# Optimization experiments

Hardware: AMD Instinct MI355X
Metric: run time of the kernel (lower is better)

The kernel has to match this reference:

```python
import jax, jax.numpy as jnp
import numpy as np

N, E = 384, 3072          # nodes, relation pairs
CIN, EMB, D = 4096, 200, 512  # roi feat dim, glove dim, hidden dim
NOBJ, NREL = 151, 51
NUM_ITER = 3
ALPHA = 0.5


def setup_inputs() -> dict:
    key = jax.random.key(0)
    ks = iter(jax.random.split(key, 64))

    def w(shape, scale=0.02):
        return jax.random.normal(next(ks), shape, dtype=jnp.float32) * scale

    inp = {
        'x': jax.random.normal(next(ks), (N, CIN), dtype=jnp.float32),
        'pos_info': jax.random.uniform(next(ks), (N, 9), dtype=jnp.float32),
        'union_features': jax.random.normal(next(ks), (E, CIN), dtype=jnp.float32),
        'obj_labels': jax.random.randint(next(ks), (N,), 0, NOBJ, dtype=jnp.int32),
        'rel_pair_idx': jax.random.randint(next(ks), (E, 2), 0, N, dtype=jnp.int32),
        # embeddings
        'obj_embed1_w': w((NOBJ, EMB)),
        'obj_embed2_w': w((NOBJ, EMB)),
        # node/edge embeddings
        'node_emb_w': w((D, CIN + EMB + 128)), 'node_emb_b': jnp.zeros((D,)),
        'node_emb2_w': w((D, CIN + EMB + D)), 'node_emb2_b': jnp.zeros((D,)),
        'edge_emb_w': w((D, CIN)), 'edge_emb_b': jnp.zeros((D,)),
        # pos_embed: Linear(9,32) -> BN(32) -> Linear(32,128) -> ReLU
        'pos_w1': w((32, 9)), 'pos_b1': jnp.zeros((32,)),
        'pos_gamma': jnp.ones((32,)), 'pos_beta': jnp.zeros((32,)),
        'pos_w2': w((128, 32)), 'pos_b2': jnp.zeros((128,)),
        # node GRUCell (with bias), edge GRUCell (no bias); gate order r,z,n
        'ngate_wih': w((3 * D, D)), 'ngate_whh': w((3 * D, D)),
        'ngate_bih': jnp.zeros((3 * D,)), 'ngate_bhh': jnp.zeros((3 * D,)),
        'egate_wih': w((3 * D, D)), 'egate_whh': w((3 * D, D)),
        # message kernels
        'n2n_w1': w((D, D)), 'n2n_b1': jnp.zeros((D,)),
        'n2n_w2': w((D, D)), 'n2n_b2': jnp.zeros((D,)),
        'e2n_w1': w((D, D)), 'e2n_b1': jnp.zeros((D,)),
        'e2n_w2': w((D, D)), 'e2n_b2': jnp.zeros((D,)),
        # node2edge 1x1 convs == pointwise linears
        'n2e_w1': w((D, 2 * D)), 'n2e_b1': jnp.zeros((D,)),
        'n2e_w2': w((D, D)), 'n2e_b2': jnp.zeros((D,)),
        'rel_cls_w': w((NREL, D)), 'rel_cls_b': jnp.zeros((NREL,)),
    }
    return inp


def _gru(x, h, wih, whh, bih=None, bhh=None):
    gi = x @ wih.T
    gh = h @ whh.T
    if bih is not None:
        gi = gi + bih
        gh = gh + bhh
    ir, iz, ig = jnp.split(gi, 3, axis=-1)
    hr, hz, hg = jnp.split(gh, 3, axis=-1)
    r = jax.nn.sigmoid(ir + hr)
    z = jax.nn.sigmoid(iz + hz)
    g = jnp.tanh(ig + r * hg)
    return (1.0 - z) * g + z * h


def _mlp2(h, w1, b1, w2, b2):
    h = jax.nn.relu(h @ w1.T + b1)
    return jax.nn.relu(h @ w2.T + b2)


def reference(x, pos_info, union_features, obj_labels, rel_pair_idx,
              obj_embed1_w, obj_embed2_w,
              node_emb_w, node_emb_b, node_emb2_w, node_emb2_b,
              edge_emb_w, edge_emb_b,
              pos_w1, pos_b1, pos_gamma, pos_beta, pos_w2, pos_b2,
              ngate_wih, ngate_whh, ngate_bih, ngate_bhh,
              egate_wih, egate_whh,
              n2n_w1, n2n_b1, n2n_w2, n2n_b2,
              e2n_w1, e2n_b1, e2n_w2, e2n_b2,
              n2e_w1, n2e_b1, n2e_w2, n2e_b2,
              rel_cls_w, rel_cls_b):
    n = x.shape[0]
    # pos embed (BatchNorm in training mode = batch stats)
    ph = pos_info @ pos_w1.T + pos_b1
    mu, var = ph.mean(0), ph.var(0)
    ph = (ph - mu) * jax.lax.rsqrt(var + 1e-5) * pos_gamma + pos_beta
    pos_embed = jax.nn.relu(ph @ pos_w2.T + pos_b2)

    obj_embed = obj_embed1_w[obj_labels]  # predcls: GT labels
    node_states = jnp.concatenate([x, obj_embed, pos_embed], -1) @ node_emb_w.T + node_emb_b

    p0, p1 = rel_pair_idx[:, 0], rel_pair_idx[:, 1]
    adj = jnp.zeros((n, n), jnp.float32).at[p0, p1].set(1.0)
    edge_rep = union_features @ edge_emb_w.T + edge_emb_b
    # torch sparse to_dense sums duplicate indices
    edge_states = jnp.zeros((n, n, D), jnp.float32).at[p0, p1].add(edge_rep)

    deg = adj.sum(1, keepdims=True) + 1e-6
    for _ in range(NUM_ITER):
        n2n = (adj @ node_states) / deg
        e2n = jnp.einsum('ij,ijd->jd', adj, edge_states)
        n2n = _mlp2(n2n, n2n_w1, n2n_b1, n2n_w2, n2n_b2)
        e2n = _mlp2(e2n, e2n_w1, e2n_b1, e2n_w2, e2n_b2)
        node_states = _gru(ALPHA * n2n + (1.0 - ALPHA) * e2n, node_states,
                           ngate_wih, ngate_whh, ngate_bih, ngate_bhh)

    # predcls: obj_dists = to_onehot(labels), preds = labels
    obj_dists = jnp.full((n, NOBJ), -1000.0, jnp.float32).at[jnp.arange(n), obj_labels].set(1000.0)
    node_states = jnp.concatenate([x, node_states, obj_embed2_w[obj_labels]], -1) @ node_emb2_w.T + node_emb2_b

    for _ in range(NUM_ITER):
        # all-pairs direction-aware concat, masked by adjacency
        ek = jnp.concatenate([
            jnp.broadcast_to(node_states[:, None, :], (n, n, D)),
            jnp.broadcast_to(node_states[None, :, :], (n, n, D)),
        ], -1) * adj[:, :, None]                      # [n, n, 2D]
        msg = _mlp2(ek, n2e_w1, n2e_b1, n2e_w2, n2e_b2)  # 1x1 convs == pointwise
        edge_states = _gru(msg.reshape(n * n, D), edge_states.reshape(n * n, D),
                           egate_wih, egate_whh).reshape(n, n, D)

    rel_feats = edge_states[p0, p1]
    rel_dists = rel_feats @ rel_cls_w.T + rel_cls_b
    return obj_dists, rel_dists
```

## Files before the change

kernel.cpp:

```cpp
#include <hip/hip_runtime.h>

typedef unsigned short ushort_t;
typedef unsigned int uint_t;

#define N_    384
#define E_    3072
#define CIN_  4096
#define EMB_  200
#define D_    512
#define NOBJ_ 151
#define NREL_ 51
#define K1_   (CIN_ + EMB_ + 128)
#define K1P_  4448
#define K2_   (CIN_ + EMB_ + D_)
#define K2P_  4832

__device__ __forceinline__ ushort_t f2b(float f) {
    uint_t u = __float_as_uint(f);
    u += 0x7FFFu + ((u >> 16) & 1u);
    return (ushort_t)(u >> 16);
}

__global__ void k_pair_min(const int* __restrict__ rp, int* __restrict__ mapMin) {
    int e = blockIdx.x * blockDim.x + threadIdx.x;
    if (e >= E_) return;
    atomicMin(&mapMin[rp[2 * e] * N_ + rp[2 * e + 1]], e);
}
__global__ void k_pair_rep(const int* __restrict__ rp, const int* __restrict__ mapMin,
                           int* __restrict__ rep, int* __restrict__ deg_cnt) {
    int e = blockIdx.x * blockDim.x + threadIdx.x;
    if (e >= E_) return;
    int r = mapMin[rp[2 * e] * N_ + rp[2 * e + 1]];
    rep[e] = r;
    if (r == e) atomicAdd(&deg_cnt[rp[2 * e]], 1);
}
__global__ void k_inv_deg(const int* __restrict__ deg_cnt, float* __restrict__ inv_deg) {
    int i = blockIdx.x * blockDim.x + threadIdx.x;
    if (i < N_) inv_deg[i] = 1.0f / ((float)deg_cnt[i] + 1e-6f);
}

__global__ __launch_bounds__(1024) void k_pos_a(const float* __restrict__ pi,
                                                const float* __restrict__ w1,
                                                const float* __restrict__ b1,
                                                const float* __restrict__ g,
                                                const float* __restrict__ be,
                                                float* __restrict__ posn) {
    __shared__ float ph[N_ * 32];
    __shared__ float mu_s[32], rs_s[32];
    int tid = threadIdx.x;
    for (int idx = tid; idx < N_ * 32; idx += 1024) {
        int i = idx >> 5, f = idx & 31;
        float s = b1[f];
        for (int k = 0; k < 9; ++k) s += pi[i * 9 + k] * w1[f * 9 + k];
        ph[idx] = s;
    }
    __syncthreads();
    if (tid < 32) {
        float s = 0.f;
        for (int i = 0; i < N_; ++i) s += ph[i * 32 + tid];
        float m = s / N_;
        float v = 0.f;
        for (int i = 0; i < N_; ++i) { float d = ph[i * 32 + tid] - m; v += d * d; }
        mu_s[tid] = m;
        rs_s[tid] = rsqrtf(v / N_ + 1e-5f);
    }
    __syncthreads();
    for (int idx = tid; idx < N_ * 32; idx += 1024) {
        int f = idx & 31;
        posn[idx] = (ph[idx] - mu_s[f]) * rs_s[f] * g[f] + be[f];
    }
}
__global__ void k_pos2(const float* __restrict__ pn, const float* __restrict__ w,
                       const float* __restrict__ b, float* __restrict__ out) {
    int idx = blockIdx.x * blockDim.x + threadIdx.x;
    if (idx >= N_ * 128) return;
    int i = idx / 128, f = idx % 128;
    float s = b[f];
    for (int k = 0; k < 32; ++k) s += pn[i * 32 + k] * w[f * 32 + k];
    out[idx] = fmaxf(s, 0.f);
}

__global__ void k_build_A1b(const float* __restrict__ x, const int* __restrict__ lab,
                            const float* __restrict__ emb1, const float* __restrict__ pe,
                            ushort_t* __restrict__ A) {
    int idx = blockIdx.x * blockDim.x + threadIdx.x;
    if (idx >= N_ * K1P_) return;
    int i = idx / K1P_, c = idx % K1P_;
    float v = 0.f;
    if (c < CIN_)             v = x[(size_t)i * CIN_ + c];
    else if (c < CIN_ + EMB_) v = emb1[lab[i] * EMB_ + (c - CIN_)];
    else if (c < K1_)         v = pe[i * 128 + (c - CIN_ - EMB_)];
    A[idx] = f2b(v);
}
__global__ void k_build_A2b(const float* __restrict__ x, const int* __restrict__ lab,
                            const float* __restrict__ emb2, const float* __restrict__ ns,
                            ushort_t* __restrict__ A) {
    int idx = blockIdx.x * blockDim.x + threadIdx.x;
    if (idx >= N_ * K2P_) return;
    int i = idx / K2P_, c = idx % K2P_;
    float v = 0.f;
    if (c < CIN_)             v = x[(size_t)i * CIN_ + c];
    else if (c < CIN_ + D_)   v = ns[i * D_ + (c - CIN_)];
    else if (c < K2_)         v = emb2[lab[i] * EMB_ + (c - CIN_ - D_)];
    A[idx] = f2b(v);
}
__global__ void k_build_ekb(const int* __restrict__ rp, const float* __restrict__ ns,
                            ushort_t* __restrict__ ek) {
    int idx = blockIdx.x * blockDim.x + threadIdx.x;
    if (idx >= E_ * 2 * D_) return;
    int e = idx / (2 * D_), c = idx % (2 * D_);
    float v = (c < D_) ? ns[rp[2 * e] * D_ + c] : ns[rp[2 * e + 1] * D_ + (c - D_)];
    ek[idx] = f2b(v);
}

struct ConvDesc { const float* src; ushort_t* dst; int K, Kp, rows, rowsp; };
struct ConvArgs { ConvDesc d[16]; };
__global__ void k_conv_batch(ConvArgs a) {
    ConvDesc c = a.d[blockIdx.y];
    for (int row = blockIdx.x; row < c.rowsp; row += gridDim.x) {
        const float* src = c.src + (size_t)row * c.K;
        ushort_t* dst = c.dst + (size_t)row * c.Kp;
        bool inrow = row < c.rows;
        for (int k = threadIdx.x * 4; k < c.Kp; k += blockDim.x * 4) {
            uint2 ov = {0u, 0u};
            if (inrow && k < c.K) {
                float4 v = *(const float4*)(src + k);
                ov.x = (uint_t)f2b(v.x) | ((uint_t)f2b(v.y) << 16);
                ov.y = (uint_t)f2b(v.z) | ((uint_t)f2b(v.w) << 16);
            }
            *(uint2*)(dst + k) = ov;
        }
    }
}
__global__ void k_f2b_n(const float* __restrict__ s, ushort_t* __restrict__ d, int n) {
    int i = blockIdx.x * blockDim.x + threadIdx.x;
    if (i < n) d[i] = f2b(s[i]);
}

__global__ void k_scatter_edge(const float* __restrict__ er, const int* __restrict__ rep,
                               float* __restrict__ es) {
    int e = blockIdx.x;
    int d = blockIdx.y * 256 + threadIdx.x;
    atomicAdd(&es[(size_t)rep[e] * D_ + d], er[(size_t)e * D_ + d]);
}
__global__ void k_broadcast_es(const int* __restrict__ rep, float* __restrict__ es,
                               ushort_t* __restrict__ esb) {
    int idx = blockIdx.x * blockDim.x + threadIdx.x;
    if (idx >= E_ * D_) return;
    int e = idx / D_, d = idx % D_;
    float v = es[(size_t)rep[e] * D_ + d];
    es[idx] = v;
    esb[idx] = f2b(v);
}
__global__ void k_scatter_e2n(const int* __restrict__ rp, const int* __restrict__ rep,
                              const float* __restrict__ es, float* __restrict__ e2n) {
    int e = blockIdx.x;
    if (rep[e] != e) return;
    int d = blockIdx.y * 256 + threadIdx.x;
    atomicAdd(&e2n[rp[2 * e + 1] * D_ + d], es[(size_t)e * D_ + d]);
}
__global__ void k_scatter_n2n(const int* __restrict__ rp, const int* __restrict__ rep,
                              const float* __restrict__ ns, float* __restrict__ n2n) {
    int e = blockIdx.x;
    if (rep[e] != e) return;
    int d = blockIdx.y * 256 + threadIdx.x;
    atomicAdd(&n2n[rp[2 * e] * D_ + d], ns[rp[2 * e + 1] * D_ + d]);
}
__global__ void k_scale_rows_b(const float* __restrict__ a, const float* __restrict__ inv_deg,
                               ushort_t* __restrict__ ob) {
    int idx = blockIdx.x * blockDim.x + threadIdx.x;
    if (idx >= N_ * D_) return;
    ob[idx] = f2b(a[idx] * inv_deg[idx / D_]);
}
__global__ void k_combine_b(const float* __restrict__ a, const float* __restrict__ b,
                            ushort_t* __restrict__ o) {
    int idx = blockIdx.x * blockDim.x + threadIdx.x;
    if (idx >= N_ * D_) return;
    o[idx] = f2b(0.5f * a[idx] + 0.5f * b[idx]);
}
__global__ void k_gru(const float* __restrict__ gi, const float* __restrict__ gh,
                      const float* __restrict__ bih, const float* __restrict__ bhh,
                      float* __restrict__ h, ushort_t* __restrict__ hb, int M) {
    int idx = blockIdx.x * blockDim.x + threadIdx.x;
    if (idx >= M * D_) return;
    int m = idx / D_, d = idx % D_;
    size_t b3 = (size_t)m * 3 * D_;
    float ir = gi[b3 + d], iz = gi[b3 + D_ + d], ig = gi[b3 + 2 * D_ + d];
    float hr = gh[b3 + d], hz = gh[b3 + D_ + d], hg = gh[b3 + 2 * D_ + d];
    if (bih) { ir += bih[d]; iz += bih[D_ + d]; ig += bih[2 * D_ + d]; }
    if (bhh) { hr += bhh[d]; hz += bhh[D_ + d]; hg += bhh[2 * D_ + d]; }
    float r = 1.f / (1.f + expf(-(ir + hr)));
    float z = 1.f / (1.f + expf(-(iz + hz)));
    float g = tanhf(ig + r * hg);
    size_t hi = (size_t)m * D_ + d;
    float nv = (1.f - z) * g + z * h[hi];
    h[hi] = nv;
    if (hb) hb[hi] = f2b(nv);
}
__global__ void k_obj_dists(const int* __restrict__ lab, float* __restrict__ out) {
    int idx = blockIdx.x * blockDim.x + threadIdx.x;
    if (idx >= N_ * NOBJ_) return;
    out[idx] = (idx % NOBJ_ == lab[idx / NOBJ_]) ? 1000.f : -1000.f;
}

typedef __attribute__((ext_vector_type(8))) short sh8;
typedef __attribute__((ext_vector_type(4))) float f32x4;

#define GLOAD_LDS16(gp, lp)                                                        \
    __builtin_amdgcn_global_load_lds((__attribute__((address_space(1))) void*)(gp),\
                                     (__attribute__((address_space(3))) void*)(lp),\
                                     16, 0, 0)

template <int FM, int FN>
__device__ __forceinline__ void gemm_body(ushort_t* As, ushort_t* Bs,
                                          const ushort_t* __restrict__ A,
                                          const ushort_t* __restrict__ B,
                                          const float* __restrict__ bias,
                                          float* __restrict__ C,
                                          ushort_t* __restrict__ Cb,
                                          int M, int N, int K, int relu,
                                          int bx, int by) {
    constexpr int BM = FM * 32, BN = FN * 32;
    constexpr int ATILES = (BM + 63) / 64, BTILES = (BN + 63) / 64;
    const int tid = threadIdx.x;
    const int lane = tid & 63, wid = tid >> 6;
    const int wr = wid >> 1, wc = wid & 1;
    const int bm = by * BM, bn = bx * BN;
    const int ar = tid >> 2, ac = (tid & 3) * 8;
    const int l15 = lane & 15, lg = lane >> 4;

    f32x4 acc[FM][FN];
#pragma unroll
    for (int m = 0; m < FM; ++m)
#pragma unroll
        for (int n = 0; n < FN; ++n) acc[m][n] = (f32x4){0.f, 0.f, 0.f, 0.f};

    for (int k0 = 0; k0 < K; k0 += 32) {
#pragma unroll
        for (int i = 0; i < ATILES; ++i) {
            int r = i * 64 + ar;
            if ((BM & 63) == 0 || r < BM)
                GLOAD_LDS16(A + (size_t)(bm + r) * K + k0 + ac, &As[r * 32 + ac]);
        }
#pragma unroll
        for (int i = 0; i < BTILES; ++i) {
            int r = i * 64 + ar;
            if ((BN & 63) == 0 || r < BN)
                GLOAD_LDS16(B + (size_t)(bn + r) * K + k0 + ac, &Bs[r * 32 + ac]);
        }
        __syncthreads();
        sh8 af[FM], bf[FN];
#pragma unroll
        for (int m = 0; m < FM; ++m)
            af[m] = *(const sh8*)&As[(wr * FM * 16 + m * 16 + l15) * 32 + lg * 8];
#pragma unroll
        for (int n = 0; n < FN; ++n)
            bf[n] = *(const sh8*)&Bs[(wc * FN * 16 + n * 16 + l15) * 32 + lg * 8];
#pragma unroll
        for (int m = 0; m < FM; ++m)
#pragma unroll
            for (int n = 0; n < FN; ++n)
                acc[m][n] = __builtin_amdgcn_mfma_f32_16x16x32_bf16(af[m], bf[n], acc[m][n], 0, 0, 0);
        __syncthreads();
    }

    const int r0 = bm + wr * FM * 16, c0 = bn + wc * FN * 16;
#pragma unroll
    for (int m = 0; m < FM; ++m)
#pragma unroll
        for (int n = 0; n < FN; ++n)
#pragma unroll
            for (int j = 0; j < 4; ++j) {
                int row = r0 + m * 16 + lg * 4 + j;
                int col = c0 + n * 16 + l15;
                if (row < M && col < N) {
                    float v = acc[m][n][j] + (bias ? bias[col] : 0.f);
                    if (relu) v = fmaxf(v, 0.f);
                    if (C)  C[(size_t)row * N + col] = v;
                    if (Cb) Cb[(size_t)row * N + col] = f2b(v);
                }
            }
}

template <int FM, int FN>
__global__ __launch_bounds__(256) void gemm_mfma(const ushort_t* __restrict__ A,
                                                 const ushort_t* __restrict__ B,
                                                 const float* __restrict__ bias,
                                                 float* __restrict__ C,
                                                 ushort_t* __restrict__ Cb,
                                                 int M, int N, int K, int relu) {
    __shared__ ushort_t As[FM * 32 * 32];
    __shared__ ushort_t Bs[FN * 32 * 32];
    gemm_body<FM, FN>(As, Bs, A, B, bias, C, Cb, M, N, K, relu, blockIdx.x, blockIdx.y);
}

__global__ __launch_bounds__(256) void gemm_dual11(const ushort_t* __restrict__ A0,
                                                   const ushort_t* __restrict__ B0,
                                                   float* __restrict__ C0,
                                                   const ushort_t* __restrict__ A1,
                                                   const ushort_t* __restrict__ B1,
                                                   float* __restrict__ C1,
                                                   int M, int N, int K) {
    __shared__ ushort_t As[32 * 32];
    __shared__ ushort_t Bs[32 * 32];
    if (blockIdx.z == 0)
        gemm_body<1, 1>(As, Bs, A0, B0, nullptr, C0, nullptr, M, N, K, 0, blockIdx.x, blockIdx.y);
    else
        gemm_body<1, 1>(As, Bs, A1, B1, nullptr, C1, nullptr, M, N, K, 0, blockIdx.x, blockIdx.y);
}

static inline dim3 mgrid(int M, int N, int FM, int FN) {
    return dim3((N + FN * 32 - 1) / (FN * 32), (M + FM * 32 - 1) / (FM * 32));
}

extern "C" void kernel_launch(void* const* d_in, const int* in_sizes, int n_in,
                              void* d_out, int out_size, void* d_ws, size_t ws_size,
                              hipStream_t stream) {
    const float* x      = (const float*)d_in[0];
    const float* posi   = (const float*)d_in[1];
    const float* unionf = (const float*)d_in[2];
    const int*   lab    = (const int*)d_in[3];
    const int*   rp     = (const int*)d_in[4];
    const float* emb1   = (const float*)d_in[5];
    const float* emb2   = (const float*)d_in[6];
    const float* nw     = (const float*)d_in[7];
    const float* nb     = (const float*)d_in[8];
    const float* nw2    = (const float*)d_in[9];
    const float* nb2    = (const float*)d_in[10];
    const float* ew     = (const float*)d_in[11];
    const float* eb     = (const float*)d_in[12];
    const float* pw1    = (const float*)d_in[13];
    const float* pb1    = (const float*)d_in[14];
    const float* pg     = (const float*)d_in[15];
    const float* pbe    = (const float*)d_in[16];
    const float* pw2    = (const float*)d_in[17];
    const float* pb2    = (const float*)d_in[18];
    const float* ngwih  = (const float*)d_in[19];
    const float* ngwhh  = (const float*)d_in[20];
    const float* ngbih  = (const float*)d_in[21];
    const float* ngbhh  = (const float*)d_in[22];
    const float* egwih  = (const float*)d_in[23];
    const float* egwhh  = (const float*)d_in[24];
    const float* n2nw1  = (const float*)d_in[25];
    const float* n2nb1  = (const float*)d_in[26];
    const float* n2nw2  = (const float*)d_in[27];
    const float* n2nb2  = (const float*)d_in[28];
    const float* e2nw1  = (const float*)d_in[29];
    const float* e2nb1  = (const float*)d_in[30];
    const float* e2nw2  = (const float*)d_in[31];
    const float* e2nb2  = (const float*)d_in[32];
    const float* n2ew1  = (const float*)d_in[33];
    const float* n2eb1  = (const float*)d_in[34];
    const float* n2ew2  = (const float*)d_in[35];
    const float* n2eb2  = (const float*)d_in[36];
    const float* relw   = (const float*)d_in[37];
    const float* relb   = (const float*)d_in[38];

    size_t off = 0;
    auto alloc = [&](size_t bytes) {
        off = (off + 255) & ~(size_t)255;
        char* p = (char*)d_ws + off;
        off += bytes;
        return (void*)p;
    };
    int*      mapMin  = (int*)alloc((size_t)N_ * N_ * 4);
    int*      rep     = (int*)alloc(E_ * 4);
    int*      deg_cnt = (int*)alloc(N_ * 4);
    float*    inv_deg = (float*)alloc(N_ * 4);
    float*    posn    = (float*)alloc(N_ * 32 * 4);
    float*    pe      = (float*)alloc(N_ * 128 * 4);
    float*    ns      = (float*)alloc((size_t)N_ * D_ * 4);
    ushort_t* nsb     = (ushort_t*)alloc((size_t)N_ * D_ * 2);
    char*     unionU  = (char*)alloc((size_t)E_ * 2 * D_ * 2);
    ushort_t* A1b = (ushort_t*)unionU;
    ushort_t* A2b = (ushort_t*)unionU;
    ushort_t* ekb = (ushort_t*)unionU;
    char*     ufbU = (char*)alloc((size_t)E_ * CIN_ * 2);
    ushort_t* ufb = (ushort_t*)ufbU;
    float*    gie = (float*)ufbU;
    char*     erepU = (char*)alloc((size_t)E_ * D_ * 4);
    float*    erep  = (float*)erepU;
    ushort_t* erepb = (ushort_t*)erepU;
    ushort_t* msgb  = (ushort_t*)(erepU + (size_t)E_ * D_ * 2);
    float*    es    = (float*)alloc((size_t)E_ * D_ * 4);
    ushort_t* esb   = (ushort_t*)alloc((size_t)E_ * D_ * 2);
    float*    e2n   = (float*)alloc((size_t)N_ * D_ * 4);
    ushort_t* e2nb  = (ushort_t*)alloc((size_t)N_ * D_ * 2);
    ushort_t* tmpb  = (ushort_t*)alloc((size_t)N_ * D_ * 2);
    float*    e2nm  = (float*)alloc((size_t)N_ * D_ * 4);
    float*    n2n   = (float*)alloc((size_t)N_ * D_ * 4);
    ushort_t* n2nb  = (ushort_t*)alloc((size_t)N_ * D_ * 2);
    float*    n2nm  = (float*)alloc((size_t)N_ * D_ * 4);
    ushort_t* xinb  = (ushort_t*)alloc((size_t)N_ * D_ * 2);
    char*     gheU = (char*)alloc((size_t)E_ * 3 * D_ * 4);
    float*    ghe = (float*)gheU;
    float*    gin = (float*)gheU;
    float*    ghn = (float*)(gheU + (size_t)N_ * 3 * D_ * 4);
    ushort_t* nwb     = (ushort_t*)alloc((size_t)D_ * K1P_ * 2);
    ushort_t* nw2b    = (ushort_t*)alloc((size_t)D_ * K2P_ * 2);
    ushort_t* ewb     = (ushort_t*)alloc((size_t)D_ * CIN_ * 2);
    ushort_t* ngwihb  = (ushort_t*)alloc((size_t)3 * D_ * D_ * 2);
    ushort_t* ngwhhb  = (ushort_t*)alloc((size_t)3 * D_ * D_ * 2);
    ushort_t* egwihb  = (ushort_t*)alloc((size_t)3 * D_ * D_ * 2);
    ushort_t* egwhhb  = (ushort_t*)alloc((size_t)3 * D_ * D_ * 2);
    ushort_t* n2nw1b  = (ushort_t*)alloc((size_t)D_ * D_ * 2);
    ushort_t* n2nw2b  = (ushort_t*)alloc((size_t)D_ * D_ * 2);
    ushort_t* e2nw1b  = (ushort_t*)alloc((size_t)D_ * D_ * 2);
    ushort_t* e2nw2b  = (ushort_t*)alloc((size_t)D_ * D_ * 2);
    ushort_t* n2ew1b  = (ushort_t*)alloc((size_t)D_ * 2 * D_ * 2);
    ushort_t* n2ew2b  = (ushort_t*)alloc((size_t)D_ * D_ * 2);
    ushort_t* relwb   = (ushort_t*)alloc((size_t)64 * D_ * 2);
    if (off > ws_size) return;

    float* out_obj = (float*)d_out;
    float* out_rel = (float*)d_out + N_ * NOBJ_;

    ConvArgs ca;
    int ci = 0;
    auto addc = [&](const float* s, ushort_t* dptr, int K, int Kp, int rows, int rowsp) {
        ca.d[ci++] = ConvDesc{s, dptr, K, Kp, rows, rowsp};
    };
    addc(nw,    nwb,    K1_,      K1P_,     D_,       D_);
    addc(nw2,   nw2b,   K2_,      K2P_,     D_,       D_);
    addc(ew,    ewb,    CIN_,     CIN_,     D_,       D_);
    addc(ngwih, ngwihb, D_,       D_,       3 * D_,   3 * D_);
    addc(ngwhh, ngwhhb, D_,       D_,       3 * D_,   3 * D_);
    addc(egwih, egwihb, D_,       D_,       3 * D_,   3 * D_);
    addc(egwhh, egwhhb, D_,       D_,       3 * D_,   3 * D_);
    addc(n2nw1, n2nw1b, D_,       D_,       D_,       D_);
    addc(n2nw2, n2nw2b, D_,       D_,       D_,       D_);
    addc(e2nw1, e2nw1b, D_,       D_,       D_,       D_);
    addc(e2nw2, e2nw2b, D_,       D_,       D_,       D_);
    addc(n2ew1, n2ew1b, 2 * D_,   2 * D_,   D_,       D_);
    addc(n2ew2, n2ew2b, D_,       D_,       D_,       D_);
    addc(relw,  relwb,  D_,       D_,       NREL_,    64);
    addc(unionf, ufb,   CIN_,     CIN_,     E_,       E_);
    for (; ci < 16;) ca.d[ci++] = ConvDesc{nullptr, nullptr, 4, 4, 0, 0};
    k_conv_batch<<<dim3(512, 15), 256, 0, stream>>>(ca);

    (void)hipMemsetAsync(mapMin, 0x7F, (size_t)N_ * N_ * 4, stream);
    (void)hipMemsetAsync(deg_cnt, 0, N_ * 4, stream);
    k_pair_min<<<(E_ + 255) / 256, 256, 0, stream>>>(rp, mapMin);
    k_pair_rep<<<(E_ + 255) / 256, 256, 0, stream>>>(rp, mapMin, rep, deg_cnt);
    k_inv_deg<<<(N_ + 255) / 256, 256, 0, stream>>>(deg_cnt, inv_deg);

    k_pos_a<<<1, 1024, 0, stream>>>(posi, pw1, pb1, pg, pbe, posn);
    k_pos2<<<(N_ * 128 + 255) / 256, 256, 0, stream>>>(posn, pw2, pb2, pe);

    k_build_A1b<<<((size_t)N_ * K1P_ + 255) / 256, 256, 0, stream>>>(x, lab, emb1, pe, A1b);
    gemm_mfma<1, 1><<<mgrid(N_, D_, 1, 1), 256, 0, stream>>>(A1b, nwb, nb, ns, nsb, N_, D_, K1P_, 0);

    gemm_mfma<2, 2><<<mgrid(E_, D_, 2, 2), 256, 0, stream>>>(ufb, ewb, eb, erep, nullptr, E_, D_, CIN_, 0);
    (void)hipMemsetAsync(es, 0, (size_t)E_ * D_ * 4, stream);
    k_scatter_edge<<<dim3(E_, 2), 256, 0, stream>>>(erep, rep, es);
    k_broadcast_es<<<(E_ * D_ + 255) / 256, 256, 0, stream>>>(rep, es, esb);

    (void)hipMemsetAsync(e2n, 0, (size_t)N_ * D_ * 4, stream);
    k_scatter_e2n<<<dim3(E_, 2), 256, 0, stream>>>(rp, rep, es, e2n);
    k_f2b_n<<<(N_ * D_ + 255) / 256, 256, 0, stream>>>(e2n, e2nb, N_ * D_);
    gemm_mfma<1, 1><<<mgrid(N_, D_, 1, 1), 256, 0, stream>>>(e2nb, e2nw1b, e2nb1, nullptr, tmpb, N_, D_, D_, 1);
    gemm_mfma<1, 1><<<mgrid(N_, D_, 1, 1), 256, 0, stream>>>(tmpb, e2nw2b, e2nb2, e2nm, nullptr, N_, D_, D_, 1);

    for (int it = 0; it < 3; ++it) {
        (void)hipMemsetAsync(n2n, 0, (size_t)N_ * D_ * 4, stream);
        k_scatter_n2n<<<dim3(E_, 2), 256, 0, stream>>>(rp, rep, ns, n2n);
        k_scale_rows_b<<<(N_ * D_ + 255) / 256, 256, 0, stream>>>(n2n, inv_deg, n2nb);
        gemm_mfma<1, 1><<<mgrid(N_, D_, 1, 1), 256, 0, stream>>>(n2nb, n2nw1b, n2nb1, nullptr, tmpb, N_, D_, D_, 1);
        gemm_mfma<1, 1><<<mgrid(N_, D_, 1, 1), 256, 0, stream>>>(tmpb, n2nw2b, n2nb2, n2nm, nullptr, N_, D_, D_, 1);
        k_combine_b<<<(N_ * D_ + 255) / 256, 256, 0, stream>>>(n2nm, e2nm, xinb);
        {
            dim3 g = mgrid(N_, 3 * D_, 1, 1);
            gemm_dual11<<<dim3(g.x, g.y, 2), 256, 0, stream>>>(xinb, ngwihb, gin, nsb, ngwhhb, ghn, N_, 3 * D_, D_);
        }
        k_gru<<<(N_ * D_ + 255) / 256, 256, 0, stream>>>(gin, ghn, ngbih, ngbhh, ns, nsb, N_);
    }

    k_obj_dists<<<(N_ * NOBJ_ + 255) / 256, 256, 0, stream>>>(lab, out_obj);

    k_build_A2b<<<((size_t)N_ * K2P_ + 255) / 256, 256, 0, stream>>>(x, lab, emb2, ns, A2b);
    gemm_mfma<1, 1><<<mgrid(N_, D_, 1, 1), 256, 0, stream>>>(A2b, nw2b, nb2, ns, nsb, N_, D_, K2P_, 0);

    k_build_ekb<<<((size_t)E_ * 2 * D_ + 255) / 256, 256, 0, stream>>>(rp, ns, ekb);
    gemm_mfma<2, 2><<<mgrid(E_, D_, 2, 2), 256, 0, stream>>>(ekb, n2ew1b, n2eb1, nullptr, erepb, E_, D_, 2 * D_, 1);
    gemm_mfma<2, 2><<<mgrid(E_, D_, 2, 2), 256, 0, stream>>>(erepb, n2ew2b, n2eb2, nullptr, msgb, E_, D_, D_, 1);
    gemm_mfma<2, 4><<<mgrid(E_, 3 * D_, 2, 4), 256, 0, stream>>>(msgb, egwihb, nullptr, gie, nullptr, E_, 3 * D_, D_, 0);
    for (int it = 0; it < 3; ++it) {
        gemm_mfma<2, 4><<<mgrid(E_, 3 * D_, 2, 4), 256, 0, stream>>>(esb, egwhhb, nullptr, ghe, nullptr, E_, 3 * D_, D_, 0);
        k_gru<<<(E_ * D_ + 255) / 256, 256, 0, stream>>>(gie, ghe, nullptr, nullptr, es, esb, E_);
    }

    gemm_mfma<1, 1><<<mgrid(E_, NREL_, 1, 1), 256, 0, stream>>>(esb, relwb, relb, out_rel, nullptr, E_, NREL_, D_, 0);
}
```

Baseline: 728.0 us.

## Apply split-K with atomic accumulation to small-M node GEMMs and add epilogue kernels

Replaces the single-pass GEMMs for the node-side linears (N=384 rows), the edge embedding, the GRU gate projections and the relation classifier with a split-K variant. Each K-slice block atomically adds its partial sum into a zeroed fp32 buffer, and separate epilogue kernels then apply bias and ReLU and write the bf16 copy. The goal is more blocks for GEMMs whose grids were too small to fill the GPU. The cost is extra memsets, fp32 atomics, extra launches and non-deterministic summation order.

```diff
diff --git a/kernel.cpp b/kernel.cpp
--- a/kernel.cpp
+++ b/kernel.cpp
@@ -172,11 +172,29 @@
     if (idx >= N_ * D_) return;
     ob[idx] = f2b(a[idx] * inv_deg[idx / D_]);
 }
-__global__ void k_combine_b(const float* __restrict__ a, const float* __restrict__ b,
-                            ushort_t* __restrict__ o) {
+__global__ void k_combine_b(const float* __restrict__ araw, const float* __restrict__ b2,
+                            const float* __restrict__ e2nm, ushort_t* __restrict__ o) {
     int idx = blockIdx.x * blockDim.x + threadIdx.x;
     if (idx >= N_ * D_) return;
-    o[idx] = f2b(0.5f * a[idx] + 0.5f * b[idx]);
+    float a = fmaxf(araw[idx] + b2[idx & (D_ - 1)], 0.f);
+    o[idx] = f2b(0.5f * a + 0.5f * e2nm[idx]);
+}
+__global__ void k_epi(const float* __restrict__ raw, const float* __restrict__ bias,
+                      float* __restrict__ fo, ushort_t* __restrict__ bo,
+                      int total, int colmask, int relu) {
+    int idx = blockIdx.x * blockDim.x + threadIdx.x;
+    if (idx >= total) return;
+    float v = raw[idx] + bias[idx & colmask];
+    if (relu) v = fmaxf(v, 0.f);
+    if (fo) fo[idx] = v;
+    if (bo) bo[idx] = f2b(v);
+}
+__global__ void k_epi_rel(const float* __restrict__ raw, const float* __restrict__ relb,
+                          float* __restrict__ out) {
+    int idx = blockIdx.x * blockDim.x + threadIdx.x;
+    if (idx >= E_ * NREL_) return;
+    int row = idx / NREL_, col = idx % NREL_;
+    out[idx] = raw[row * 64 + col] + relb[col];
 }
 __global__ void k_gru(const float* __restrict__ gi, const float* __restrict__ gh,
                       const float* __restrict__ bih, const float* __restrict__ bhh,
@@ -212,30 +230,20 @@
                                      16, 0, 0)
 
 template <int FM, int FN>
-__device__ __forceinline__ void gemm_body(ushort_t* As, ushort_t* Bs,
-                                          const ushort_t* __restrict__ A,
-                                          const ushort_t* __restrict__ B,
-                                          const float* __restrict__ bias,
-                                          float* __restrict__ C,
-                                          ushort_t* __restrict__ Cb,
-                                          int M, int N, int K, int relu,
-                                          int bx, int by) {
+__device__ __forceinline__ void gemm_kloop(ushort_t* As, ushort_t* Bs,
+                                           const ushort_t* __restrict__ A,
+                                           const ushort_t* __restrict__ B,
+                                           f32x4 (&acc)[FM][FN],
+                                           int K, int ks0, int ks1, int bm, int bn) {
     constexpr int BM = FM * 32, BN = FN * 32;
     constexpr int ATILES = (BM + 63) / 64, BTILES = (BN + 63) / 64;
     const int tid = threadIdx.x;
     const int lane = tid & 63, wid = tid >> 6;
     const int wr = wid >> 1, wc = wid & 1;
-    const int bm = by * BM, bn = bx * BN;
     const int ar = tid >> 2, ac = (tid & 3) * 8;
     const int l15 = lane & 15, lg = lane >> 4;
-
-    f32x4 acc[FM][FN];
-#pragma unroll
-    for (int m = 0; m < FM; ++m)
-#pragma unroll
-        for (int n = 0; n < FN; ++n) acc[m][n] = (f32x4){0.f, 0.f, 0.f, 0.f};
-
-    for (int k0 = 0; k0 < K; k0 += 32) {
+    for (int ks = ks0; ks < ks1; ++ks) {
+        int k0 = ks * 32;
 #pragma unroll
         for (int i = 0; i < ATILES; ++i) {
             int r = i * 64 + ar;
@@ -263,8 +271,27 @@
                 acc[m][n] = __builtin_amdgcn_mfma_f32_16x16x32_bf16(af[m], bf[n], acc[m][n], 0, 0, 0);
         __syncthreads();
     }
-
-    const int r0 = bm + wr * FM * 16, c0 = bn + wc * FN * 16;
+}
+
+template <int FM, int FN>
+__global__ __launch_bounds__(256) void gemm_mfma(const ushort_t* __restrict__ A,
+                                                 const ushort_t* __restrict__ B,
+                                                 const float* __restrict__ bias,
+                                                 float* __restrict__ C,
+                                                 ushort_t* __restrict__ Cb,
+                                                 int M, int N, int K, int relu) {
+    __shared__ ushort_t As[FM * 32 * 32];
+    __shared__ ushort_t Bs[FN * 32 * 32];
+    const int bm = blockIdx.y * FM * 32, bn = blockIdx.x * FN * 32;
+    f32x4 acc[FM][FN];
+#pragma unroll
+    for (int m = 0; m < FM; ++m)
+#pragma unroll
+        for (int n = 0; n < FN; ++n) acc[m][n] = (f32x4){0.f, 0.f, 0.f, 0.f};
+    gemm_kloop<FM, FN>(As, Bs, A, B, acc, K, 0, K / 32, bm, bn);
+    const int lane = threadIdx.x & 63, wid = threadIdx.x >> 6;
+    const int l15 = lane & 15, lg = lane >> 4;
+    const int r0 = bm + (wid >> 1) * FM * 16, c0 = bn + (wid & 1) * FN * 16;
 #pragma unroll
     for (int m = 0; m < FM; ++m)
 #pragma unroll
@@ -283,34 +310,46 @@
 }
 
 template <int FM, int FN>
-__global__ __launch_bounds__(256) void gemm_mfma(const ushort_t* __restrict__ A,
-                                                 const ushort_t* __restrict__ B,
-                                                 const float* __restrict__ bias,
-                                                 float* __restrict__ C,
-                                                 ushort_t* __restrict__ Cb,
-                                                 int M, int N, int K, int relu) {
+__global__ __launch_bounds__(256) void gemm_splitk(const ushort_t* __restrict__ A,
+                                                   const ushort_t* __restrict__ B,
+                                                   float* __restrict__ C,
+                                                   int M, int N, int K, int S) {
     __shared__ ushort_t As[FM * 32 * 32];
     __shared__ ushort_t Bs[FN * 32 * 32];
-    gemm_body<FM, FN>(As, Bs, A, B, bias, C, Cb, M, N, K, relu, blockIdx.x, blockIdx.y);
-}
-
-__global__ __launch_bounds__(256) void gemm_dual11(const ushort_t* __restrict__ A0,
-                                                   const ushort_t* __restrict__ B0,
-                                                   float* __restrict__ C0,
-                                                   const ushort_t* __restrict__ A1,
-                                                   const ushort_t* __restrict__ B1,
-                                                   float* __restrict__ C1,
-                                                   int M, int N, int K) {
-    __shared__ ushort_t As[32 * 32];
-    __shared__ ushort_t Bs[32 * 32];
-    if (blockIdx.z == 0)
-        gemm_body<1, 1>(As, Bs, A0, B0, nullptr, C0, nullptr, M, N, K, 0, blockIdx.x, blockIdx.y);
-    else
-        gemm_body<1, 1>(As, Bs, A1, B1, nullptr, C1, nullptr, M, N, K, 0, blockIdx.x, blockIdx.y);
+    const int nsteps = K / 32;
+    const int ss = (nsteps + S - 1) / S;
+    const int ks0 = blockIdx.z * ss;
+    const int ks1 = min(nsteps, ks0 + ss);
+    if (ks0 >= ks1) return;
+    const int bm = blockIdx.y * FM * 32, bn = blockIdx.x * FN * 32;
+    f32x4 acc[FM][FN];
+#pragma unroll
+    for (int m = 0; m < FM; ++m)
+#pragma unroll
+        for (int n = 0; n < FN; ++n) acc[m][n] = (f32x4){0.f, 0.f, 0.f, 0.f};
+    gemm_kloop<FM, FN>(As, Bs, A, B, acc, K, ks0, ks1, bm, bn);
+    const int lane = threadIdx.x & 63, wid = threadIdx.x >> 6;
+    const int l15 = lane & 15, lg = lane >> 4;
+    const int r0 = bm + (wid >> 1) * FM * 16, c0 = bn + (wid & 1) * FN * 16;
+#pragma unroll
+    for (int m = 0; m < FM; ++m)
+#pragma unroll
+        for (int n = 0; n < FN; ++n)
+#pragma unroll
+            for (int j = 0; j < 4; ++j) {
+                int row = r0 + m * 16 + lg * 4 + j;
+                int col = c0 + n * 16 + l15;
+                if (row < M && col < N)
+                    atomicAdd(&C[(size_t)row * N + col], acc[m][n][j]);
+            }
 }
 
 static inline dim3 mgrid(int M, int N, int FM, int FN) {
     return dim3((N + FN * 32 - 1) / (FN * 32), (M + FM * 32 - 1) / (FM * 32));
+}
+static inline dim3 sgrid(int M, int N, int FM, int FN, int S) {
+    dim3 g = mgrid(M, N, FM, FN);
+    return dim3(g.x, g.y, S);
 }
 
 extern "C" void kernel_launch(void* const* d_in, const int* in_sizes, int n_in,
@@ -371,6 +410,16 @@
     float*    pe      = (float*)alloc(N_ * 128 * 4);
     float*    ns      = (float*)alloc((size_t)N_ * D_ * 4);
     ushort_t* nsb     = (ushort_t*)alloc((size_t)N_ * D_ * 2);
+    float*    nsraw   = (float*)alloc((size_t)N_ * D_ * 4);
+    char*     scrR    = (char*)alloc((size_t)(2 * N_ * D_ + N_ * D_ + 2 * N_ * 3 * D_) * 4);
+    float*    n2n     = (float*)scrR;
+    float*    tmpraw  = (float*)(scrR + (size_t)N_ * D_ * 4);
+    float*    n2nmraw = (float*)(scrR + (size_t)2 * N_ * D_ * 4);
+    float*    gin     = (float*)(scrR + (size_t)3 * N_ * D_ * 4);
+    float*    ghn     = (float*)(scrR + (size_t)(3 * N_ * D_ + N_ * 3 * D_) * 4);
+    const size_t scrBytes = (size_t)(3 * N_ * D_ + 2 * N_ * 3 * D_) * 4;
+    float*    e2nm    = (float*)alloc((size_t)N_ * D_ * 4);
+    float*    relraw  = (float*)alloc((size_t)E_ * 64 * 4);
     char*     unionU  = (char*)alloc((size_t)E_ * 2 * D_ * 2);
     ushort_t* A1b = (ushort_t*)unionU;
     ushort_t* A2b = (ushort_t*)unionU;
@@ -387,15 +436,9 @@
     float*    e2n   = (float*)alloc((size_t)N_ * D_ * 4);
     ushort_t* e2nb  = (ushort_t*)alloc((size_t)N_ * D_ * 2);
     ushort_t* tmpb  = (ushort_t*)alloc((size_t)N_ * D_ * 2);
-    float*    e2nm  = (float*)alloc((size_t)N_ * D_ * 4);
-    float*    n2n   = (float*)alloc((size_t)N_ * D_ * 4);
     ushort_t* n2nb  = (ushort_t*)alloc((size_t)N_ * D_ * 2);
-    float*    n2nm  = (float*)alloc((size_t)N_ * D_ * 4);
     ushort_t* xinb  = (ushort_t*)alloc((size_t)N_ * D_ * 2);
-    char*     gheU = (char*)alloc((size_t)E_ * 3 * D_ * 4);
-    float*    ghe = (float*)gheU;
-    float*    gin = (float*)gheU;
-    float*    ghn = (float*)(gheU + (size_t)N_ * 3 * D_ * 4);
+    float*    ghe   = (float*)alloc((size_t)E_ * 3 * D_ * 4);
     ushort_t* nwb     = (ushort_t*)alloc((size_t)D_ * K1P_ * 2);
     ushort_t* nw2b    = (ushort_t*)alloc((size_t)D_ * K2P_ * 2);
     ushort_t* ewb     = (ushort_t*)alloc((size_t)D_ * CIN_ * 2);
@@ -448,9 +491,13 @@
     k_pos2<<<(N_ * 128 + 255) / 256, 256, 0, stream>>>(posn, pw2, pb2, pe);
 
     k_build_A1b<<<((size_t)N_ * K1P_ + 255) / 256, 256, 0, stream>>>(x, lab, emb1, pe, A1b);
-    gemm_mfma<1, 1><<<mgrid(N_, D_, 1, 1), 256, 0, stream>>>(A1b, nwb, nb, ns, nsb, N_, D_, K1P_, 0);
-
-    gemm_mfma<2, 2><<<mgrid(E_, D_, 2, 2), 256, 0, stream>>>(ufb, ewb, eb, erep, nullptr, E_, D_, CIN_, 0);
+    (void)hipMemsetAsync(nsraw, 0, (size_t)N_ * D_ * 4, stream);
+    gemm_splitk<1, 1><<<sgrid(N_, D_, 1, 1, 8), 256, 0, stream>>>(A1b, nwb, nsraw, N_, D_, K1P_, 8);
+    k_epi<<<(N_ * D_ + 255) / 256, 256, 0, stream>>>(nsraw, nb, ns, nsb, N_ * D_, D_ - 1, 0);
+
+    (void)hipMemsetAsync(erep, 0, (size_t)E_ * D_ * 4, stream);
+    gemm_splitk<2, 2><<<sgrid(E_, D_, 2, 2, 2), 256, 0, stream>>>(ufb, ewb, erep, E_, D_, CIN_, 2);
+    k_epi<<<((size_t)E_ * D_ + 255) / 256, 256, 0, stream>>>(erep, eb, erep, nullptr, E_ * D_, D_ - 1, 0);
     (void)hipMemsetAsync(es, 0, (size_t)E_ * D_ * 4, stream);
     k_scatter_edge<<<dim3(E_, 2), 256, 0, stream>>>(erep, rep, es);
     k_broadcast_es<<<(E_ * D_ + 255) / 256, 256, 0, stream>>>(rep, es, esb);
@@ -458,27 +505,31 @@
     (void)hipMemsetAsync(e2n, 0, (size_t)N_ * D_ * 4, stream);
     k_scatter_e2n<<<dim3(E_, 2), 256, 0, stream>>>(rp, rep, es, e2n);
     k_f2b_n<<<(N_ * D_ + 255) / 256, 256, 0, stream>>>(e2n, e2nb, N_ * D_);
-    gemm_mfma<1, 1><<<mgrid(N_, D_, 1, 1), 256, 0, stream>>>(e2nb, e2nw1b, e2nb1, nullptr, tmpb, N_, D_, D_, 1);
-    gemm_mfma<1, 1><<<mgrid(N_, D_, 1, 1), 256, 0, stream>>>(tmpb, e2nw2b, e2nb2, e2nm, nullptr, N_, D_, D_, 1);
+    (void)hipMemsetAsync(scrR, 0, scrBytes, stream);
+    gemm_splitk<1, 1><<<sgrid(N_, D_, 1, 1, 8), 256, 0, stream>>>(e2nb, e2nw1b, tmpraw, N_, D_, D_, 8);
+    k_epi<<<(N_ * D_ + 255) / 256, 256, 0, stream>>>(tmpraw, e2nb1, nullptr, tmpb, N_ * D_, D_ - 1, 1);
+    gemm_splitk<1, 1><<<sgrid(N_, D_, 1, 1, 8), 256, 0, stream>>>(tmpb, e2nw2b, n2nmraw, N_, D_, D_, 8);
+    k_epi<<<(N_ * D_ + 255) / 256, 256, 0, stream>>>(n2nmraw, e2nb2, e2nm, nullptr, N_ * D_, D_ - 1, 1);
 
     for (int it = 0; it < 3; ++it) {
-        (void)hipMemsetAsync(n2n, 0, (size_t)N_ * D_ * 4, stream);
+        (void)hipMemsetAsync(scrR, 0, scrBytes, stream);
         k_scatter_n2n<<<dim3(E_, 2), 256, 0, stream>>>(rp, rep, ns, n2n);
         k_scale_rows_b<<<(N_ * D_ + 255) / 256, 256, 0, stream>>>(n2n, inv_deg, n2nb);
-        gemm_mfma<1, 1><<<mgrid(N_, D_, 1, 1), 256, 0, stream>>>(n2nb, n2nw1b, n2nb1, nullptr, tmpb, N_, D_, D_, 1);
-        gemm_mfma<1, 1><<<mgrid(N_, D_, 1, 1), 256, 0, stream>>>(tmpb, n2nw2b, n2nb2, n2nm, nullptr, N_, D_, D_, 1);
-        k_combine_b<<<(N_ * D_ + 255) / 256, 256, 0, stream>>>(n2nm, e2nm, xinb);
-        {
-            dim3 g = mgrid(N_, 3 * D_, 1, 1);
-            gemm_dual11<<<dim3(g.x, g.y, 2), 256, 0, stream>>>(xinb, ngwihb, gin, nsb, ngwhhb, ghn, N_, 3 * D_, D_);
-        }
+        gemm_splitk<1, 1><<<sgrid(N_, D_, 1, 1, 8), 256, 0, stream>>>(n2nb, n2nw1b, tmpraw, N_, D_, D_, 8);
+        k_epi<<<(N_ * D_ + 255) / 256, 256, 0, stream>>>(tmpraw, n2nb1, nullptr, tmpb, N_ * D_, D_ - 1, 1);
+        gemm_splitk<1, 1><<<sgrid(N_, D_, 1, 1, 8), 256, 0, stream>>>(tmpb, n2nw2b, n2nmraw, N_, D_, D_, 8);
+        k_combine_b<<<(N_ * D_ + 255) / 256, 256, 0, stream>>>(n2nmraw, n2nb2, e2nm, xinb);
+        gemm_splitk<1, 1><<<sgrid(N_, 3 * D_, 1, 1, 4), 256, 0, stream>>>(xinb, ngwihb, gin, N_, 3 * D_, D_, 4);
+        gemm_splitk<1, 1><<<sgrid(N_, 3 * D_, 1, 1, 4), 256, 0, stream>>>(nsb, ngwhhb, ghn, N_, 3 * D_, D_, 4);
         k_gru<<<(N_ * D_ + 255) / 256, 256, 0, stream>>>(gin, ghn, ngbih, ngbhh, ns, nsb, N_);
     }
 
     k_obj_dists<<<(N_ * NOBJ_ + 255) / 256, 256, 0, stream>>>(lab, out_obj);
 
     k_build_A2b<<<((size_t)N_ * K2P_ + 255) / 256, 256, 0, stream>>>(x, lab, emb2, ns, A2b);
-    gemm_mfma<1, 1><<<mgrid(N_, D_, 1, 1), 256, 0, stream>>>(A2b, nw2b, nb2, ns, nsb, N_, D_, K2P_, 0);
+    (void)hipMemsetAsync(nsraw, 0, (size_t)N_ * D_ * 4, stream);
+    gemm_splitk<1, 1><<<sgrid(N_, D_, 1, 1, 8), 256, 0, stream>>>(A2b, nw2b, nsraw, N_, D_, K2P_, 8);
+    k_epi<<<(N_ * D_ + 255) / 256, 256, 0, stream>>>(nsraw, nb2, ns, nsb, N_ * D_, D_ - 1, 0);
 
     k_build_ekb<<<((size_t)E_ * 2 * D_ + 255) / 256, 256, 0, stream>>>(rp, ns, ekb);
     gemm_mfma<2, 2><<<mgrid(E_, D_, 2, 2), 256, 0, stream>>>(ekb, n2ew1b, n2eb1, nullptr, erepb, E_, D_, 2 * D_, 1);
@@ -489,5 +540,7 @@
         k_gru<<<(E_ * D_ + 255) / 256, 256, 0, stream>>>(gie, ghe, nullptr, nullptr, es, esb, E_);
     }
 
-    gemm_mfma<1, 1><<<mgrid(E_, NREL_, 1, 1), 256, 0, stream>>>(esb, relwb, relb, out_rel, nullptr, E_, NREL_, D_, 0);
-}
+    (void)hipMemsetAsync(relraw, 0, (size_t)E_ * 64 * 4, stream);
+    gemm_splitk<1, 1><<<sgrid(E_, 64, 1, 1, 4), 256, 0, stream>>>(esb, relwb, relraw, E_, 64, D_, 4);
+    k_epi_rel<<<(E_ * NREL_ + 255) / 256, 256, 0, stream>>>(relraw, relb, out_rel);
+}
```

Result: faster. 705.0 us (-3.2%).
